# Kernel optimization log

Hardware: AMD Instinct MI355X
Metric: run time of the kernel (lower is better)

The kernel has to match this reference:

```python
import jax, jax.numpy as jnp
import numpy as np
import math

N = 16384        # nodes / rows of inputs
DIN = 256        # input_dimension
DOUT = 64        # output_dimension (contraction dim of second matmul)
M = 16384        # columns of normalized_adjacency (output width)


def setup_inputs() -> dict:
    key = jax.random.key(0)
    k1, k2, k3 = jax.random.split(key, 3)
    inputs = jax.random.normal(k1, (N, DIN), dtype=jnp.float32)
    normalized_adjacency = jax.random.uniform(k2, (DOUT, M), dtype=jnp.float32)
    dev = 1.0 / math.sqrt(DOUT)  # Xavier-style uniform init from source
    weights = jax.random.uniform(k3, (DIN, DOUT), dtype=jnp.float32,
                                 minval=-dev, maxval=dev)
    return {"inputs": inputs, "normalized_adjacency": normalized_adjacency,
            "weights": weights}


def reference(inputs, normalized_adjacency, weights):
    # before = X @ W : [N, DOUT]
    before = jnp.matmul(inputs, weights)
    # returning = before @ A : [N, M]  (spmm in source; same math densely)
    returning = jnp.matmul(before, normalized_adjacency)
    # bias=0 => no bias add; torch legacy softmax on 2-D uses dim=1
    return jax.nn.softmax(returning, axis=-1)
```

## Files before the change

### kernel.cpp

```cpp
#include <hip/hip_runtime.h>
#include <hip/hip_bf16.h>

#define N_ROWS 16384
#define DIN_K  256
#define DOUT_K 64
#define M_COLS 16384
#define LOG2E  1.4426950408889634f

typedef __attribute__((ext_vector_type(8))) short short8;
typedef __attribute__((ext_vector_type(4))) float f32x4;

#define MFMA16 __builtin_amdgcn_mfma_f32_16x16x32_bf16
#define EXP2F  __builtin_amdgcn_exp2f
#define LOG2F  __builtin_amdgcn_logf

__device__ inline unsigned short f32_bf16_rne(float x) {
    unsigned u = __builtin_bit_cast(unsigned, x);
    u += 0x7fffu + ((u >> 16) & 1u);
    return (unsigned short)(u >> 16);
}
__device__ inline float bf16_f32(unsigned short h) {
    unsigned u = ((unsigned)h) << 16;
    return __builtin_bit_cast(float, u);
}

__global__ __launch_bounds__(256) void k_before(
    const float* __restrict__ X, const float* __restrict__ W,
    float* __restrict__ off2,
    unsigned short* __restrict__ bh, unsigned short* __restrict__ bl)
{
    const int row  = blockIdx.x * 4 + (threadIdx.x >> 6);
    const int lane = threadIdx.x & 63;
    const float* xr = X + (size_t)row * DIN_K;
    float acc = 0.f;
    #pragma unroll 8
    for (int d = 0; d < DIN_K; ++d)
        acc = fmaf(xr[d], W[d * DOUT_K + lane], acc);
    const float bs = acc * LOG2E;
    const unsigned short hs = f32_bf16_rne(bs);
    const float hf = bf16_f32(hs);
    const unsigned short ls = f32_bf16_rne(bs - hf);
    bh[row * DOUT_K + lane] = hs;
    bl[row * DOUT_K + lane] = ls;
    float t = fmaxf(bs, 0.f);
    #pragma unroll
    for (int m = 1; m < 64; m <<= 1) t += __shfl_xor(t, m, 64);
    if (lane == 0) off2[row] = t;
}

__global__ __launch_bounds__(256) void k_pack(
    const float* __restrict__ A,
    unsigned short* __restrict__ ahp, unsigned short* __restrict__ alp)
{
    const int wid   = blockIdx.x * 4 + (threadIdx.x >> 6);
    const int lane  = threadIdx.x & 63;
    const int chunk = wid >> 1, ks = wid & 1;
    const int col   = chunk * 16 + (lane & 15);
    const int kb    = ks * 32 + ((lane >> 4) * 8);
    const size_t base = ((size_t)(chunk * 2 + ks) * 64 + lane) * 8;
    #pragma unroll
    for (int i = 0; i < 8; ++i) {
        const float a = A[(size_t)(kb + i) * M_COLS + col];
        const unsigned short hs = f32_bf16_rne(a);
        ahp[base + i] = hs;
        alp[base + i] = f32_bf16_rne(a - bf16_f32(hs));
    }
}

__global__ __launch_bounds__(512, 2) void k_main(
    const unsigned short* __restrict__ bh, const unsigned short* __restrict__ bl,
    const unsigned short* __restrict__ ahp, const unsigned short* __restrict__ alp,
    const float* __restrict__ off2, float* __restrict__ out)
{
    __shared__ float lds[8][64];
    __shared__ float sout0[64 * 260];
    __shared__ float sout1[64 * 260];
    const int wave = threadIdx.x >> 6;
    const int lane = threadIdx.x & 63;
    const int lrow = lane & 15;
    const int lgrp = lane >> 4;
    const int r0   = blockIdx.x * 64;
    const int rot  = (((blockIdx.x << 3) | wave) * 53) & 127;
    const int cbase = wave * 128;

#define CIDX(j) (cbase + (((j) + rot) & 127))

    short8 bHf[4][2], bLf[4][2];
    #pragma unroll
    for (int rt = 0; rt < 4; ++rt)
        #pragma unroll
        for (int ks = 0; ks < 2; ++ks) {
            const size_t o = (size_t)(r0 + rt * 16 + lrow) * DOUT_K + ks * 32 + lgrp * 8;
            bHf[rt][ks] = *reinterpret_cast<const short8*>(bh + o);
            bLf[rt][ks] = *reinterpret_cast<const short8*>(bl + o);
        }

    float negoff[4];
    #pragma unroll
    for (int rt = 0; rt < 4; ++rt)
        negoff[rt] = -off2[r0 + rt * 16 + lrow];

    float lsum[4] = {0.f, 0.f, 0.f, 0.f};

#define LOADA(H0, H1, c) {                                                  \
    const size_t _b = (size_t)((c) * 2) * 512 + lane * 8;                   \
    H0 = *reinterpret_cast<const short8*>(ahp + _b);                        \
    H1 = *reinterpret_cast<const short8*>(ahp + _b + 512); }

#define LOADB(H0, H1, L0, L1, c) {                                          \
    const size_t _b = (size_t)((c) * 2) * 512 + lane * 8;                   \
    H0 = *reinterpret_cast<const short8*>(ahp + _b);                        \
    H1 = *reinterpret_cast<const short8*>(ahp + _b + 512);                  \
    L0 = *reinterpret_cast<const short8*>(alp + _b);                        \
    L1 = *reinterpret_cast<const short8*>(alp + _b + 512); }

#define BODY1(H0, H1)                                                       \
    _Pragma("unroll")                                                       \
    for (int rt = 0; rt < 4; ++rt) {                                        \
        f32x4 acc = { negoff[rt], negoff[rt], negoff[rt], negoff[rt] };     \
        acc = MFMA16(H0, bHf[rt][0], acc, 0, 0, 0);                         \
        acc = MFMA16(H1, bHf[rt][1], acc, 0, 0, 0);                         \
        acc = MFMA16(H0, bLf[rt][0], acc, 0, 0, 0);                         \
        acc = MFMA16(H1, bLf[rt][1], acc, 0, 0, 0);                         \
        lsum[rt] += (EXP2F(acc[0]) + EXP2F(acc[1]))                         \
                  + (EXP2F(acc[2]) + EXP2F(acc[3])); }

    short8 cH0, cH1, nH0, nH1;

    LOADA(cH0, cH1, CIDX(0));
    for (int j = 0; j < 128; j += 2) {
        LOADA(nH0, nH1, CIDX(j + 1));
        BODY1(cH0, cH1);
        LOADA(cH0, cH1, CIDX(j + 2));
        BODY1(nH0, nH1);
    }

    #pragma unroll
    for (int rt = 0; rt < 4; ++rt) {
        float v = lsum[rt];
        v += __shfl_xor(v, 16, 64);
        v += __shfl_xor(v, 32, 64);
        lsum[rt] = v;
    }
    if (lgrp == 0) {
        #pragma unroll
        for (int rt = 0; rt < 4; ++rt)
            lds[wave][rt * 16 + lrow] = lsum[rt];
    }
    __syncthreads();

    float base2[4];
    #pragma unroll
    for (int rt = 0; rt < 4; ++rt) {
        const int rl = rt * 16 + lrow;
        float tot = ((lds[0][rl] + lds[1][rl]) + (lds[2][rl] + lds[3][rl]))
                  + ((lds[4][rl] + lds[5][rl]) + (lds[6][rl] + lds[7][rl]));
        base2[rt] = negoff[rt] - LOG2F(tot);
    }

    const int rotb = (blockIdx.x * 37) & 63;
    const int k0 = wave * 2, k1 = wave * 2 + 1;

#define LOADPAIR(H00,H01,L00,L01, H10,H11,L10,L11, sp) {                    \
    const int _cc = (sp) * 16 + k0;                                         \
    LOADB(H00, H01, L00, L01, _cc);                                         \
    LOADB(H10, H11, L10, L11, _cc + 1); }

#define BODY2L(H0, H1, L0, L1, kk, BUF)                                     \
    _Pragma("unroll")                                                       \
    for (int rt = 0; rt < 4; ++rt) {                                        \
        f32x4 acc = { base2[rt], base2[rt], base2[rt], base2[rt] };         \
        acc = MFMA16(H0, bHf[rt][0], acc, 0, 0, 0);                         \
        acc = MFMA16(H1, bHf[rt][1], acc, 0, 0, 0);                         \
        acc = MFMA16(L0, bHf[rt][0], acc, 0, 0, 0);                         \
        acc = MFMA16(L1, bHf[rt][1], acc, 0, 0, 0);                         \
        acc = MFMA16(H0, bLf[rt][0], acc, 0, 0, 0);                         \
        acc = MFMA16(H1, bLf[rt][1], acc, 0, 0, 0);                         \
        f32x4 o4 = { EXP2F(acc[0]), EXP2F(acc[1]),                          \
                     EXP2F(acc[2]), EXP2F(acc[3]) };                        \
        *reinterpret_cast<f32x4*>(                                          \
            &BUF[(rt * 16 + lrow) * 260 + (kk) * 16 + lgrp * 4]) = o4; }

#define STOREPHASE(sp, BUF) {                                               \
    const size_t _cb = (size_t)(sp) * 256;                                  \
    _Pragma("unroll")                                                       \
    for (int i = 0; i < 8; ++i) {                                           \
        const int _rw = wave * 8 + i;                                       \
        const f32x4 v = *reinterpret_cast<const f32x4*>(                    \
            &BUF[_rw * 260 + lane * 4]);                                    \
        __builtin_nontemporal_store(v, reinterpret_cast<f32x4*>(            \
            out + (size_t)(r0 + _rw) * M_COLS + _cb + lane * 4)); } }

    short8 A0H0,A0H1,A0L0,A0L1, A1H0,A1H1,A1L0,A1L1;
    short8 B0H0,B0H1,B0L0,B0L1, B1H0,B1H1,B1L0,B1L1;

    LOADPAIR(A0H0,A0H1,A0L0,A0L1, A1H0,A1H1,A1L0,A1L1, rotb);
    BODY2L(A0H0,A0H1,A0L0,A0L1, k0, sout0);
    BODY2L(A1H0,A1H1,A1L0,A1L1, k1, sout0);
    LOADPAIR(B0H0,B0H1,B0L0,B0L1, B1H0,B1H1,B1L0,B1L1, (1 + rotb) & 63);
    __syncthreads();

    for (int s = 0; s < 62; s += 2) {
        const int spE = (s + rotb) & 63;
        const int spO = (s + 1 + rotb) & 63;
        STOREPHASE(spE, sout0);
        LOADPAIR(A0H0,A0H1,A0L0,A0L1, A1H0,A1H1,A1L0,A1L1, (s + 2 + rotb) & 63);
        BODY2L(B0H0,B0H1,B0L0,B0L1, k0, sout1);
        BODY2L(B1H0,B1H1,B1L0,B1L1, k1, sout1);
        __syncthreads();
        STOREPHASE(spO, sout1);
        LOADPAIR(B0H0,B0H1,B0L0,B0L1, B1H0,B1H1,B1L0,B1L1, (s + 3 + rotb) & 63);
        BODY2L(A0H0,A0H1,A0L0,A0L1, k0, sout0);
        BODY2L(A1H0,A1H1,A1L0,A1L1, k1, sout0);
        __syncthreads();
    }
    STOREPHASE((62 + rotb) & 63, sout0);
    BODY2L(B0H0,B0H1,B0L0,B0L1, k0, sout1);
    BODY2L(B1H0,B1H1,B1L0,B1L1, k1, sout1);
    __syncthreads();
    STOREPHASE((63 + rotb) & 63, sout1);
#undef CIDX
#undef LOADA
#undef LOADB
#undef BODY1
#undef LOADPAIR
#undef BODY2L
#undef STOREPHASE
}

extern "C" void kernel_launch(void* const* d_in, const int* in_sizes, int n_in,
                              void* d_out, int out_size, void* d_ws, size_t ws_size,
                              hipStream_t stream) {
    const float* X = (const float*)d_in[0];
    const float* A = (const float*)d_in[1];
    const float* W = (const float*)d_in[2];
    float* out = (float*)d_out;

    char* wsb = (char*)d_ws;
    float*          off2 = (float*)wsb;
    unsigned short* bh   = (unsigned short*)(wsb + (1u << 16));
    unsigned short* bl   = (unsigned short*)(wsb + (1u << 16) + (1u << 21));
    unsigned short* ahp  = (unsigned short*)(wsb + (1u << 16) + 2u * (1u << 21));
    unsigned short* alp  = (unsigned short*)(wsb + (1u << 16) + 3u * (1u << 21));

    hipLaunchKernelGGL(k_before, dim3(N_ROWS / 4), dim3(256), 0, stream, X, W, off2, bh, bl);
    hipLaunchKernelGGL(k_pack,   dim3(512),        dim3(256), 0, stream, A, ahp, alp);
    hipLaunchKernelGGL(k_main,   dim3(256),        dim3(512), 0, stream, bh, bl, ahp, alp, off2, out);
}
```

Before: 307.9 us.

## Split softmax denominator pass into separate wider-grid kernel with partial sums

Moves the first pass, which sums exponentials for the softmax denominator, out of the main kernel into its own kernel. That kernel runs 1024 blocks of 256 threads, each covering a quarter of the columns, and writes per-column-group partial sums to workspace. The final kernel sums the four partials per row and does only the second pass with its output stores. The aim is to lift the low occupancy of the 256-block main kernel during the compute-bound denominator pass, at the cost of an extra launch and reloading the B fragments.

```diff
diff --git a/kernel.cpp b/kernel.cpp
--- a/kernel.cpp
+++ b/kernel.cpp
@@ -67,23 +67,23 @@
     }
 }
 
-__global__ __launch_bounds__(512, 2) void k_main(
+__global__ __launch_bounds__(256, 4) void k_denom(
     const unsigned short* __restrict__ bh, const unsigned short* __restrict__ bl,
-    const unsigned short* __restrict__ ahp, const unsigned short* __restrict__ alp,
-    const float* __restrict__ off2, float* __restrict__ out)
-{
-    __shared__ float lds[8][64];
-    __shared__ float sout0[64 * 260];
-    __shared__ float sout1[64 * 260];
+    const unsigned short* __restrict__ ahp,
+    const float* __restrict__ off2, float* __restrict__ partial)
+{
+    __shared__ float lds[4][64];
     const int wave = threadIdx.x >> 6;
     const int lane = threadIdx.x & 63;
     const int lrow = lane & 15;
     const int lgrp = lane >> 4;
-    const int r0   = blockIdx.x * 64;
-    const int rot  = (((blockIdx.x << 3) | wave) * 53) & 127;
-    const int cbase = wave * 128;
-
-#define CIDX(j) (cbase + (((j) + rot) & 127))
+    const int cg   = blockIdx.x & 3;
+    const int rb   = blockIdx.x >> 2;
+    const int r0   = rb * 64;
+    const int cbase = cg * 256 + wave * 64;
+    const int rot  = (((blockIdx.x << 2) | wave) * 53) & 63;
+
+#define CIDX(j) (cbase + (((j) + rot) & 63))
 
     short8 bHf[4][2], bLf[4][2];
     #pragma unroll
@@ -106,13 +106,6 @@
     const size_t _b = (size_t)((c) * 2) * 512 + lane * 8;                   \
     H0 = *reinterpret_cast<const short8*>(ahp + _b);                        \
     H1 = *reinterpret_cast<const short8*>(ahp + _b + 512); }
-
-#define LOADB(H0, H1, L0, L1, c) {                                          \
-    const size_t _b = (size_t)((c) * 2) * 512 + lane * 8;                   \
-    H0 = *reinterpret_cast<const short8*>(ahp + _b);                        \
-    H1 = *reinterpret_cast<const short8*>(ahp + _b + 512);                  \
-    L0 = *reinterpret_cast<const short8*>(alp + _b);                        \
-    L1 = *reinterpret_cast<const short8*>(alp + _b + 512); }
 
 #define BODY1(H0, H1)                                                       \
     _Pragma("unroll")                                                       \
@@ -126,14 +119,16 @@
                   + (EXP2F(acc[2]) + EXP2F(acc[3])); }
 
     short8 cH0, cH1, nH0, nH1;
-
     LOADA(cH0, cH1, CIDX(0));
-    for (int j = 0; j < 128; j += 2) {
+    for (int j = 0; j < 64; j += 2) {
         LOADA(nH0, nH1, CIDX(j + 1));
         BODY1(cH0, cH1);
         LOADA(cH0, cH1, CIDX(j + 2));
         BODY1(nH0, nH1);
     }
+#undef CIDX
+#undef LOADA
+#undef BODY1
 
     #pragma unroll
     for (int rt = 0; rt < 4; ++rt) {
@@ -148,18 +143,55 @@
             lds[wave][rt * 16 + lrow] = lsum[rt];
     }
     __syncthreads();
+    if (wave == 0) {
+        const float tot = (lds[0][lane] + lds[1][lane])
+                        + (lds[2][lane] + lds[3][lane]);
+        partial[(size_t)cg * N_ROWS + r0 + lane] = tot;
+    }
+}
+
+__global__ __launch_bounds__(512, 2) void k_final(
+    const unsigned short* __restrict__ bh, const unsigned short* __restrict__ bl,
+    const unsigned short* __restrict__ ahp, const unsigned short* __restrict__ alp,
+    const float* __restrict__ off2, const float* __restrict__ partial,
+    float* __restrict__ out)
+{
+    __shared__ float sout0[64 * 260];
+    __shared__ float sout1[64 * 260];
+    const int wave = threadIdx.x >> 6;
+    const int lane = threadIdx.x & 63;
+    const int lrow = lane & 15;
+    const int lgrp = lane >> 4;
+    const int r0   = blockIdx.x * 64;
+
+    short8 bHf[4][2], bLf[4][2];
+    #pragma unroll
+    for (int rt = 0; rt < 4; ++rt)
+        #pragma unroll
+        for (int ks = 0; ks < 2; ++ks) {
+            const size_t o = (size_t)(r0 + rt * 16 + lrow) * DOUT_K + ks * 32 + lgrp * 8;
+            bHf[rt][ks] = *reinterpret_cast<const short8*>(bh + o);
+            bLf[rt][ks] = *reinterpret_cast<const short8*>(bl + o);
+        }
 
     float base2[4];
     #pragma unroll
     for (int rt = 0; rt < 4; ++rt) {
-        const int rl = rt * 16 + lrow;
-        float tot = ((lds[0][rl] + lds[1][rl]) + (lds[2][rl] + lds[3][rl]))
-                  + ((lds[4][rl] + lds[5][rl]) + (lds[6][rl] + lds[7][rl]));
-        base2[rt] = negoff[rt] - LOG2F(tot);
-    }
+        const int row = r0 + rt * 16 + lrow;
+        const float tot = (partial[row] + partial[N_ROWS + row])
+                        + (partial[2 * N_ROWS + row] + partial[3 * N_ROWS + row]);
+        base2[rt] = -off2[row] - LOG2F(tot);
+    }
+
+#define LOADB(H0, H1, L0, L1, c) {                                          \
+    const size_t _b = (size_t)((c) * 2) * 512 + lane * 8;                   \
+    H0 = *reinterpret_cast<const short8*>(ahp + _b);                        \
+    H1 = *reinterpret_cast<const short8*>(ahp + _b + 512);                  \
+    L0 = *reinterpret_cast<const short8*>(alp + _b);                        \
+    L1 = *reinterpret_cast<const short8*>(alp + _b + 512); }
 
     const int rotb = (blockIdx.x * 37) & 63;
-    const int k0 = wave * 2, k1 = wave * 2 + 1;
+    const int k0 = wave * 2;
 
 #define LOADPAIR(H00,H01,L00,L01, H10,H11,L10,L11, sp) {                    \
     const int _cc = (sp) * 16 + k0;                                         \
@@ -196,7 +228,7 @@
 
     LOADPAIR(A0H0,A0H1,A0L0,A0L1, A1H0,A1H1,A1L0,A1L1, rotb);
     BODY2L(A0H0,A0H1,A0L0,A0L1, k0, sout0);
-    BODY2L(A1H0,A1H1,A1L0,A1L1, k1, sout0);
+    BODY2L(A1H0,A1H1,A1L0,A1L1, k0 + 1, sout0);
     LOADPAIR(B0H0,B0H1,B0L0,B0L1, B1H0,B1H1,B1L0,B1L1, (1 + rotb) & 63);
     __syncthreads();
 
@@ -206,23 +238,20 @@
         STOREPHASE(spE, sout0);
         LOADPAIR(A0H0,A0H1,A0L0,A0L1, A1H0,A1H1,A1L0,A1L1, (s + 2 + rotb) & 63);
         BODY2L(B0H0,B0H1,B0L0,B0L1, k0, sout1);
-        BODY2L(B1H0,B1H1,B1L0,B1L1, k1, sout1);
+        BODY2L(B1H0,B1H1,B1L0,B1L1, k0 + 1, sout1);
         __syncthreads();
         STOREPHASE(spO, sout1);
         LOADPAIR(B0H0,B0H1,B0L0,B0L1, B1H0,B1H1,B1L0,B1L1, (s + 3 + rotb) & 63);
         BODY2L(A0H0,A0H1,A0L0,A0L1, k0, sout0);
-        BODY2L(A1H0,A1H1,A1L0,A1L1, k1, sout0);
+        BODY2L(A1H0,A1H1,A1L0,A1L1, k0 + 1, sout0);
         __syncthreads();
     }
     STOREPHASE((62 + rotb) & 63, sout0);
     BODY2L(B0H0,B0H1,B0L0,B0L1, k0, sout1);
-    BODY2L(B1H0,B1H1,B1L0,B1L1, k1, sout1);
+    BODY2L(B1H0,B1H1,B1L0,B1L1, k0 + 1, sout1);
     __syncthreads();
     STOREPHASE((63 + rotb) & 63, sout1);
-#undef CIDX
-#undef LOADA
 #undef LOADB
-#undef BODY1
 #undef LOADPAIR
 #undef BODY2L
 #undef STOREPHASE
@@ -237,13 +266,15 @@
     float* out = (float*)d_out;
 
     char* wsb = (char*)d_ws;
-    float*          off2 = (float*)wsb;
-    unsigned short* bh   = (unsigned short*)(wsb + (1u << 16));
-    unsigned short* bl   = (unsigned short*)(wsb + (1u << 16) + (1u << 21));
-    unsigned short* ahp  = (unsigned short*)(wsb + (1u << 16) + 2u * (1u << 21));
-    unsigned short* alp  = (unsigned short*)(wsb + (1u << 16) + 3u * (1u << 21));
+    float*          off2    = (float*)wsb;
+    unsigned short* bh      = (unsigned short*)(wsb + (1u << 16));
+    unsigned short* bl      = (unsigned short*)(wsb + (1u << 16) + 1u * (1u << 21));
+    unsigned short* ahp     = (unsigned short*)(wsb + (1u << 16) + 2u * (1u << 21));
+    unsigned short* alp     = (unsigned short*)(wsb + (1u << 16) + 3u * (1u << 21));
+    float*          partial = (float*)(wsb + (1u << 16) + 4u * (1u << 21));
 
     hipLaunchKernelGGL(k_before, dim3(N_ROWS / 4), dim3(256), 0, stream, X, W, off2, bh, bl);
     hipLaunchKernelGGL(k_pack,   dim3(512),        dim3(256), 0, stream, A, ahp, alp);
-    hipLaunchKernelGGL(k_main,   dim3(256),        dim3(512), 0, stream, bh, bl, ahp, alp, off2, out);
-}
+    hipLaunchKernelGGL(k_denom,  dim3(1024),       dim3(256), 0, stream, bh, bl, ahp, off2, partial);
+    hipLaunchKernelGGL(k_final,  dim3(256),        dim3(512), 0, stream, bh, bl, ahp, alp, off2, partial, out);
+}
```

After: 315.1 us. +2.3%, slower.
